# Performance work log

Hardware: AMD Instinct MI355X
Metric: run time of the kernel (lower is better)

Reference implementation:

```python
import jax, jax.numpy as jnp
import numpy as np

# Sampled-neighborhood sizes (NeighborSampler-style shrinking hops)
N0, N1, N2, N3 = 200000, 50000, 12500, 3200
E0, E1, E2 = 500000, 125000, 32000
D_IN, D_H, D_OUT = 128, 256, 128


def setup_inputs() -> dict:
    key = jax.random.key(0)
    ks = jax.random.split(key, 16)
    x = jax.random.normal(ks[0], (N0, D_IN), dtype=jnp.float32)
    src0 = jax.random.randint(ks[1], (E0,), 0, N0)
    dst0 = jax.random.randint(ks[2], (E0,), 0, N1)
    src1 = jax.random.randint(ks[3], (E1,), 0, N1)
    dst1 = jax.random.randint(ks[4], (E1,), 0, N2)
    src2 = jax.random.randint(ks[5], (E2,), 0, N2)
    dst2 = jax.random.randint(ks[6], (E2,), 0, N3)
    s = 0.05
    # SAGEConv params: lin_l (applied to aggregated neighbors, has bias), lin_r (root)
    wl0 = jax.random.normal(ks[7], (D_H, D_IN), dtype=jnp.float32) * s
    wr0 = jax.random.normal(ks[8], (D_H, D_IN), dtype=jnp.float32) * s
    b0 = jnp.zeros((D_H,), dtype=jnp.float32)
    wl1 = jax.random.normal(ks[9], (D_H, D_H), dtype=jnp.float32) * s
    wr1 = jax.random.normal(ks[10], (D_H, D_H), dtype=jnp.float32) * s
    b1 = jnp.zeros((D_H,), dtype=jnp.float32)
    wl2 = jax.random.normal(ks[11], (D_OUT, D_H), dtype=jnp.float32) * s
    wr2 = jax.random.normal(ks[12], (D_OUT, D_H), dtype=jnp.float32) * s
    b2 = jnp.zeros((D_OUT,), dtype=jnp.float32)
    return {"x": x, "src0": src0, "dst0": dst0, "src1": src1, "dst1": dst1,
            "src2": src2, "dst2": dst2,
            "wl0": wl0, "wr0": wr0, "b0": b0,
            "wl1": wl1, "wr1": wr1, "b1": b1,
            "wl2": wl2, "wr2": wr2, "b2": b2}


def _sage(x, src, dst, n_tgt, wl, wr, b):
    """Bipartite SAGEConv with mean aggregation (PyG default)."""
    x_tgt = x[:n_tgt]                                   # [n_tgt, d_in]
    msg = x[src]                                        # [E, d_in] gather
    s = jax.ops.segment_sum(msg, dst, num_segments=n_tgt)
    cnt = jax.ops.segment_sum(jnp.ones((src.shape[0], 1), x.dtype), dst,
                              num_segments=n_tgt)
    mean = s / jnp.maximum(cnt, 1.0)                    # mean over in-neighbors
    return mean @ wl.T + b + x_tgt @ wr.T               # [n_tgt, d_out]


def reference(x, src0, dst0, src1, dst1, src2, dst2,
              wl0, wr0, b0, wl1, wr1, b1, wl2, wr2, b2):
    h = jax.nn.relu(_sage(x, src0, dst0, N1, wl0, wr0, b0))
    h = jax.nn.relu(_sage(h, src1, dst1, N2, wl1, wr1, b1))
    return _sage(h, src2, dst2, N3, wl2, wr2, b2)       # [N3, D_OUT]
```

## Files before the change

kernel.cpp:

```cpp
#include <hip/hip_runtime.h>

#define N0s 200000
#define N1s 50000
#define N2s 12500
#define N3s 3200
#define E0s 500000
#define E1s 125000
#define E2s 32000
#define D_INs 128
#define D_Hs 256
#define D_OUTs 128

#define CAP 64
#define LOGCAP 6

#define GSTRIDE 72

#define XS4 (N1s * D_INs / 4)
#define WN4 65536
#define CSMALL_TOTAL (XS4 + WN4)
#define CSMALL_BLOCKS ((CSMALL_TOTAL + 2047) / 2048)

typedef __attribute__((ext_vector_type(8))) short short8;
typedef __attribute__((ext_vector_type(8))) unsigned short ushort8;
typedef __attribute__((ext_vector_type(4))) float floatx4;

__device__ __forceinline__ unsigned short f32_to_bf16_rne(float f) {
    unsigned int u = __float_as_uint(f);
    u += 0x7fffu + ((u >> 16) & 1u);
    return (unsigned short)(u >> 16);
}
__device__ __forceinline__ float bf16_to_f32(unsigned short h) {
    return __uint_as_float(((unsigned int)h) << 16);
}

struct Bins {
    const int *src0, *dst0, *src1, *dst1, *src2, *dst2;
    int *cnt0, *cnt1, *cnt2;
    int *eidx0, *eidx1, *eidx2;
};

__launch_bounds__(256)
__global__ void fill3(Bins b)
{
    int e = blockIdx.x * 256 + threadIdx.x;
    if (e < E0s) {
        int d = b.dst0[e];
        int p = atomicAdd(&b.cnt0[d], 1);
        if (p < CAP) b.eidx0[(d << LOGCAP) + p] = b.src0[e];
    } else if (e < E0s + E1s) {
        int i = e - E0s;
        int d = b.dst1[i];
        int p = atomicAdd(&b.cnt1[d], 1);
        if (p < CAP) b.eidx1[(d << LOGCAP) + p] = b.src1[i];
    } else if (e < E0s + E1s + E2s) {
        int i = e - E0s - E1s;
        int d = b.dst2[i];
        int p = atomicAdd(&b.cnt2[d], 1);
        if (p < CAP) b.eidx2[(d << LOGCAP) + p] = b.src2[i];
    }
}

struct CastArgs {
    const float* x; unsigned short* xb;
    const float* ws_[6]; unsigned short* wd[6];
};

__launch_bounds__(256)
__global__ void cast_small(CastArgs a)
{
    #pragma unroll
    for (int j = 0; j < 8; ++j) {
        int i = blockIdx.x * 2048 + j * 256 + threadIdx.x;
        if (i < XS4) {
            float4 v = *(const float4*)&a.x[(size_t)i * 4];
            ushort4 o;
            o.x = f32_to_bf16_rne(v.x);
            o.y = f32_to_bf16_rne(v.y);
            o.z = f32_to_bf16_rne(v.z);
            o.w = f32_to_bf16_rne(v.w);
            *(ushort4*)&a.xb[(size_t)i * 4] = o;
        } else if (i < CSMALL_TOTAL) {
            int g = i - XS4;
            int seg, base;
            if      (g < 8192)  { seg = 0; base = 0; }
            else if (g < 16384) { seg = 1; base = 8192; }
            else if (g < 32768) { seg = 2; base = 16384; }
            else if (g < 49152) { seg = 3; base = 32768; }
            else if (g < 57344) { seg = 4; base = 49152; }
            else                { seg = 5; base = 57344; }
            int k = g - base;
            float4 v = *(const float4*)&a.ws_[seg][(size_t)k * 4];
            ushort4 o;
            o.x = f32_to_bf16_rne(v.x);
            o.y = f32_to_bf16_rne(v.y);
            o.z = f32_to_bf16_rne(v.z);
            o.w = f32_to_bf16_rne(v.w);
            *(ushort4*)&a.wd[seg][(size_t)k * 4] = o;
        }
    }
}

__launch_bounds__(256)
__global__ void gather_mean_f32(const float* __restrict__ X,
                                const int* __restrict__ eidx,
                                const int* __restrict__ cnt,
                                unsigned short* __restrict__ out,
                                int n_tgt)
{
    int gid = blockIdx.x * 256 + threadIdx.x;
    int row = gid >> 5;
    if (row >= n_tgt) return;
    int c = (gid & 31) << 2;

    int deg = cnt[row];
    int e = min(deg, CAP);
    const int* bp = &eidx[row << LOGCAP];

    float a0 = 0.f, a1 = 0.f, a2 = 0.f, a3 = 0.f;
    int i = 0;
    for (; i + 4 <= e; i += 4) {
        int4 ss = *(const int4*)&bp[i];
        float4 v0 = *(const float4*)&X[(size_t)ss.x * D_INs + c];
        float4 v1 = *(const float4*)&X[(size_t)ss.y * D_INs + c];
        float4 v2 = *(const float4*)&X[(size_t)ss.z * D_INs + c];
        float4 v3 = *(const float4*)&X[(size_t)ss.w * D_INs + c];
        a0 += (v0.x + v1.x) + (v2.x + v3.x);
        a1 += (v0.y + v1.y) + (v2.y + v3.y);
        a2 += (v0.z + v1.z) + (v2.z + v3.z);
        a3 += (v0.w + v1.w) + (v2.w + v3.w);
    }
    for (; i < e; ++i) {
        float4 v = *(const float4*)&X[(size_t)bp[i] * D_INs + c];
        a0 += v.x; a1 += v.y; a2 += v.z; a3 += v.w;
    }
    float inv = 1.0f / fmaxf((float)deg, 1.0f);
    ushort4 o;
    o.x = f32_to_bf16_rne(a0 * inv);
    o.y = f32_to_bf16_rne(a1 * inv);
    o.z = f32_to_bf16_rne(a2 * inv);
    o.w = f32_to_bf16_rne(a3 * inv);
    *(ushort4*)&out[(size_t)row * D_INs + c] = o;
}

__launch_bounds__(256)
__global__ void gather_mean(const unsigned short* __restrict__ X,
                            const int* __restrict__ eidx,
                            const int* __restrict__ cnt,
                            unsigned short* __restrict__ out,
                            int n_tgt, int D, int shift)
{
    int gid = blockIdx.x * 256 + threadIdx.x;
    int row = gid >> shift;
    if (row >= n_tgt) return;
    int c = (gid & ((1 << shift) - 1)) << 3;

    int deg = cnt[row];
    int e = min(deg, CAP);
    const int* bp = &eidx[row << LOGCAP];

    float acc[8];
    #pragma unroll
    for (int j = 0; j < 8; ++j) acc[j] = 0.f;

    int i = 0;
    for (; i + 4 <= e; i += 4) {
        int4 ss = *(const int4*)&bp[i];
        ushort8 v0 = *(const ushort8*)&X[(size_t)ss.x * D + c];
        ushort8 v1 = *(const ushort8*)&X[(size_t)ss.y * D + c];
        ushort8 v2 = *(const ushort8*)&X[(size_t)ss.z * D + c];
        ushort8 v3 = *(const ushort8*)&X[(size_t)ss.w * D + c];
        #pragma unroll
        for (int j = 0; j < 8; ++j)
            acc[j] += (bf16_to_f32(v0[j]) + bf16_to_f32(v1[j]))
                    + (bf16_to_f32(v2[j]) + bf16_to_f32(v3[j]));
    }
    for (; i < e; ++i) {
        ushort8 v0 = *(const ushort8*)&X[(size_t)bp[i] * D + c];
        #pragma unroll
        for (int j = 0; j < 8; ++j) acc[j] += bf16_to_f32(v0[j]);
    }

    float inv = 1.0f / fmaxf((float)deg, 1.0f);
    ushort8 o;
    #pragma unroll
    for (int j = 0; j < 8; ++j) o[j] = f32_to_bf16_rne(acc[j] * inv);
    *(ushort8*)&out[(size_t)row * D + c] = o;
}

template<int BM, int BN, int OUT_BF16, int RELU>
__launch_bounds__(256)
__global__ void mfma_gemm_t(const unsigned short* __restrict__ A1,
                            const unsigned short* __restrict__ A2,
                            const unsigned short* __restrict__ W1,
                            const unsigned short* __restrict__ W2,
                            const float* __restrict__ bias,
                            void* __restrict__ Cout,
                            int M, int N, int K1, int K2)
{
    constexpr int MT = BM / 32;
    constexpr int NT = BN / 32;
    constexpr int AITER = BM / 32;
    constexpr int CS = BN + 4;

    __shared__ unsigned short smem[2 * BM * GSTRIDE];
    unsigned short* As = smem;
    unsigned short* Bs = smem + BM * GSTRIDE;

    const int tid  = threadIdx.x;
    const int wave = tid >> 6;
    const int lane = tid & 63;
    const int quad = lane >> 4;
    const int lr   = lane & 15;
    const int wm   = wave >> 1;
    const int wn   = wave & 1;
    const int row0 = blockIdx.x * BM;
    const int col0 = blockIdx.y * BN;

    floatx4 acc[MT][NT] = {};

    for (int seg = 0; seg < 2; ++seg) {
        const unsigned short* Ap = (seg == 0) ? A1 : A2;
        const unsigned short* Wp = (seg == 0) ? W1 : W2;
        const int K = (seg == 0) ? K1 : K2;

        for (int k0 = 0; k0 < K; k0 += 64) {
            #pragma unroll
            for (int it = 0; it < AITER; ++it) {
                int sid = tid + it * 256;
                int r = sid >> 3;
                int sc = (sid & 7) << 3;
                int gr = min(row0 + r, M - 1);
                uint4 v = *(const uint4*)&Ap[(size_t)gr * K + k0 + sc];
                *(uint4*)&As[r * GSTRIDE + sc] = v;
            }
            #pragma unroll
            for (int it = 0; it < AITER; ++it) {
                int sid = tid + it * 256;
                int r = sid >> 3;
                int sc = (sid & 7) << 3;
                uint4 v = *(const uint4*)&Wp[(size_t)(col0 + r) * K + k0 + sc];
                *(uint4*)&Bs[r * GSTRIDE + sc] = v;
            }
            __syncthreads();

            #pragma unroll
            for (int kh = 0; kh < 2; ++kh) {
                short8 afr[MT], bfr[NT];
                #pragma unroll
                for (int mt = 0; mt < MT; ++mt)
                    afr[mt] = *(const short8*)&As[(wm * (BM/2) + mt * 16 + lr) * GSTRIDE + kh * 32 + quad * 8];
                #pragma unroll
                for (int nt = 0; nt < NT; ++nt)
                    bfr[nt] = *(const short8*)&Bs[(wn * (BN/2) + nt * 16 + lr) * GSTRIDE + kh * 32 + quad * 8];

                #pragma unroll
                for (int mt = 0; mt < MT; ++mt)
                    #pragma unroll
                    for (int nt = 0; nt < NT; ++nt)
                        acc[mt][nt] = __builtin_amdgcn_mfma_f32_16x16x32_bf16(
                            afr[mt], bfr[nt], acc[mt][nt], 0, 0, 0);
            }
            __syncthreads();
        }
    }

    if (OUT_BF16) {
        unsigned short* Cs = smem;
        #pragma unroll
        for (int nt = 0; nt < NT; ++nt) {
            int col = wn * (BN/2) + nt * 16 + lr;
            float bv = bias[col0 + col];
            #pragma unroll
            for (int mt = 0; mt < MT; ++mt) {
                #pragma unroll
                for (int reg = 0; reg < 4; ++reg) {
                    int row = wm * (BM/2) + mt * 16 + quad * 4 + reg;
                    float v = acc[mt][nt][reg] + bv;
                    if (RELU) v = fmaxf(v, 0.f);
                    Cs[row * CS + col] = f32_to_bf16_rne(v);
                }
            }
        }
        __syncthreads();
        constexpr int TPRO = 256 / BM;
        constexpr int SPT  = BN / TPRO;
        int r  = tid / TPRO;
        int hf = tid % TPRO;
        int gr = row0 + r;
        if (gr < M) {
            unsigned short* Crow = (unsigned short*)Cout + (size_t)gr * N + col0 + hf * SPT;
            #pragma unroll
            for (int j = 0; j < SPT / 8; ++j) {
                uint4 v = *(const uint4*)&Cs[r * CS + hf * SPT + j * 8];
                *(uint4*)&Crow[j * 8] = v;
            }
        }
    } else {
        #pragma unroll
        for (int nt = 0; nt < NT; ++nt) {
            int gc = col0 + wn * (BN/2) + nt * 16 + lr;
            float bv = bias[gc];
            #pragma unroll
            for (int mt = 0; mt < MT; ++mt) {
                #pragma unroll
                for (int reg = 0; reg < 4; ++reg) {
                    int gr = row0 + wm * (BM/2) + mt * 16 + quad * 4 + reg;
                    if (gr < M) {
                        float v = acc[mt][nt][reg] + bv;
                        if (RELU) v = fmaxf(v, 0.f);
                        ((float*)Cout)[(size_t)gr * N + gc] = v;
                    }
                }
            }
        }
    }
}

extern "C" void kernel_launch(void* const* d_in, const int* in_sizes, int n_in,
                              void* d_out, int out_size, void* d_ws, size_t ws_size,
                              hipStream_t stream)
{
    const float* x   = (const float*)d_in[0];
    const int* src0  = (const int*)d_in[1];
    const int* dst0  = (const int*)d_in[2];
    const int* src1  = (const int*)d_in[3];
    const int* dst1  = (const int*)d_in[4];
    const int* src2  = (const int*)d_in[5];
    const int* dst2  = (const int*)d_in[6];
    const float* wl0 = (const float*)d_in[7];
    const float* wr0 = (const float*)d_in[8];
    const float* b0  = (const float*)d_in[9];
    const float* wl1 = (const float*)d_in[10];
    const float* wr1 = (const float*)d_in[11];
    const float* b1  = (const float*)d_in[12];
    const float* wl2 = (const float*)d_in[13];
    const float* wr2 = (const float*)d_in[14];
    const float* b2  = (const float*)d_in[15];

    unsigned short* ws = (unsigned short*)d_ws;
    unsigned short* xb    = ws;
    unsigned short* h1    = xb + (size_t)N0s * D_INs;
    unsigned short* h2    = h1 + (size_t)N1s * D_Hs;
    unsigned short* meanA = h2 + (size_t)N2s * D_Hs;
    unsigned short* wl0b  = meanA + (size_t)N1s * D_INs;
    unsigned short* wr0b  = wl0b + 32768;
    unsigned short* wl1b  = wr0b + 32768;
    unsigned short* wr1b  = wl1b + 65536;
    unsigned short* wl2b  = wr1b + 65536;
    unsigned short* wr2b  = wl2b + 32768;
    int* ib = (int*)(wr2b + 32768);
    int* cnt0 = ib;
    int* cnt1 = cnt0 + 50048;
    int* cnt2 = cnt1 + 12544;
    int* eidx0 = cnt2 + 3264;
    int* eidx1 = eidx0 + (size_t)N1s * CAP;
    int* eidx2 = eidx1 + (size_t)N2s * CAP;

    Bins b;
    b.src0 = src0; b.dst0 = dst0; b.src1 = src1; b.dst1 = dst1;
    b.src2 = src2; b.dst2 = dst2;
    b.cnt0 = cnt0; b.cnt1 = cnt1; b.cnt2 = cnt2;
    b.eidx0 = eidx0; b.eidx1 = eidx1; b.eidx2 = eidx2;

    CastArgs ca;
    ca.x = x; ca.xb = xb;
    ca.ws_[0] = wl0; ca.ws_[1] = wr0; ca.ws_[2] = wl1;
    ca.ws_[3] = wr1; ca.ws_[4] = wl2; ca.ws_[5] = wr2;
    ca.wd[0] = wl0b; ca.wd[1] = wr0b; ca.wd[2] = wl1b;
    ca.wd[3] = wr1b; ca.wd[4] = wl2b; ca.wd[5] = wr2b;

    hipMemsetAsync(cnt0, 0, (50048 + 12544 + 3264) * sizeof(int), stream);
    const int Etot = E0s + E1s + E2s;
    fill3<<<(Etot + 255) / 256, 256, 0, stream>>>(b);
    cast_small<<<CSMALL_BLOCKS, 256, 0, stream>>>(ca);

    {
        int th = N1s * 32;
        gather_mean_f32<<<(th + 255) / 256, 256, 0, stream>>>(x, eidx0, cnt0,
                                                              meanA, N1s);
        dim3 g((N1s + 127) / 128, D_Hs / 128);
        mfma_gemm_t<128,128,1,1><<<g, 256, 0, stream>>>(meanA, xb, wl0b, wr0b, b0, h1,
                                                        N1s, D_Hs, D_INs, D_INs);
    }
    {
        int th = N2s * 32;
        gather_mean<<<(th + 255) / 256, 256, 0, stream>>>(h1, eidx1, cnt1,
                                                          meanA, N2s, D_Hs, 5);
        dim3 g((N2s + 63) / 64, D_Hs / 64);
        mfma_gemm_t<64,64,1,1><<<g, 256, 0, stream>>>(meanA, h1, wl1b, wr1b, b1, h2,
                                                      N2s, D_Hs, D_Hs, D_Hs);
    }
    {
        int th = N3s * 32;
        gather_mean<<<(th + 255) / 256, 256, 0, stream>>>(h2, eidx2, cnt2,
                                                          meanA, N3s, D_Hs, 5);
        dim3 g((N3s + 63) / 64, D_OUTs / 64);
        mfma_gemm_t<64,64,0,0><<<g, 256, 0, stream>>>(meanA, h2, wl2b, wr2b, b2, (float*)d_out,
                                                      N3s, D_OUTs, D_Hs, D_Hs);
    }
}
```

Before: 317.9 us.

## Fuse cast with layer-0 gather and widen GEMM tiles to full output width

Merges the bf16 cast kernel and the fp32 layer-0 gather-mean into one launch, splitting the grid between the two jobs, so one launch and one serialization point go away and the two can overlap. The GEMM template now supports BN different from BM, with separate A and B load iteration counts and shared memory sized to the max of the staging buffers and the output tile. Each layer's GEMM uses a full-width N tile (128x256, 64x256, 32x128), so the A operand is read once instead of once per column block. Wider tiles use more registers and shared memory and launch fewer blocks, which may lower occupancy, most of all on the small later layers.

```diff
diff --git a/kernel.cpp b/kernel.cpp
--- a/kernel.cpp
+++ b/kernel.cpp
@@ -20,6 +20,7 @@
 #define WN4 65536
 #define CSMALL_TOTAL (XS4 + WN4)
 #define CSMALL_BLOCKS ((CSMALL_TOTAL + 2047) / 2048)
+#define G0_BLOCKS (N1s * 32 / 256)
 
 typedef __attribute__((ext_vector_type(8))) short short8;
 typedef __attribute__((ext_vector_type(8))) unsigned short ushort8;
@@ -61,77 +62,73 @@
     }
 }
 
-struct CastArgs {
+struct G0Args {
     const float* x; unsigned short* xb;
     const float* ws_[6]; unsigned short* wd[6];
+    const int* eidx0; const int* cnt0; unsigned short* meanA;
 };
 
 __launch_bounds__(256)
-__global__ void cast_small(CastArgs a)
+__global__ void gather0_cast(G0Args a)
 {
-    #pragma unroll
-    for (int j = 0; j < 8; ++j) {
-        int i = blockIdx.x * 2048 + j * 256 + threadIdx.x;
-        if (i < XS4) {
-            float4 v = *(const float4*)&a.x[(size_t)i * 4];
-            ushort4 o;
-            o.x = f32_to_bf16_rne(v.x);
-            o.y = f32_to_bf16_rne(v.y);
-            o.z = f32_to_bf16_rne(v.z);
-            o.w = f32_to_bf16_rne(v.w);
-            *(ushort4*)&a.xb[(size_t)i * 4] = o;
-        } else if (i < CSMALL_TOTAL) {
-            int g = i - XS4;
-            int seg, base;
-            if      (g < 8192)  { seg = 0; base = 0; }
-            else if (g < 16384) { seg = 1; base = 8192; }
-            else if (g < 32768) { seg = 2; base = 16384; }
-            else if (g < 49152) { seg = 3; base = 32768; }
-            else if (g < 57344) { seg = 4; base = 49152; }
-            else                { seg = 5; base = 57344; }
-            int k = g - base;
-            float4 v = *(const float4*)&a.ws_[seg][(size_t)k * 4];
-            ushort4 o;
-            o.x = f32_to_bf16_rne(v.x);
-            o.y = f32_to_bf16_rne(v.y);
-            o.z = f32_to_bf16_rne(v.z);
-            o.w = f32_to_bf16_rne(v.w);
-            *(ushort4*)&a.wd[seg][(size_t)k * 4] = o;
+    if (blockIdx.x < CSMALL_BLOCKS) {
+        #pragma unroll
+        for (int j = 0; j < 8; ++j) {
+            int i = blockIdx.x * 2048 + j * 256 + threadIdx.x;
+            if (i < XS4) {
+                float4 v = *(const float4*)&a.x[(size_t)i * 4];
+                ushort4 o;
+                o.x = f32_to_bf16_rne(v.x);
+                o.y = f32_to_bf16_rne(v.y);
+                o.z = f32_to_bf16_rne(v.z);
+                o.w = f32_to_bf16_rne(v.w);
+                *(ushort4*)&a.xb[(size_t)i * 4] = o;
+            } else if (i < CSMALL_TOTAL) {
+                int g = i - XS4;
+                int seg, base;
+                if      (g < 8192)  { seg = 0; base = 0; }
+                else if (g < 16384) { seg = 1; base = 8192; }
+                else if (g < 32768) { seg = 2; base = 16384; }
+                else if (g < 49152) { seg = 3; base = 32768; }
+                else if (g < 57344) { seg = 4; base = 49152; }
+                else                { seg = 5; base = 57344; }
+                int k = g - base;
+                float4 v = *(const float4*)&a.ws_[seg][(size_t)k * 4];
+                ushort4 o;
+                o.x = f32_to_bf16_rne(v.x);
+                o.y = f32_to_bf16_rne(v.y);
+                o.z = f32_to_bf16_rne(v.z);
+                o.w = f32_to_bf16_rne(v.w);
+                *(ushort4*)&a.wd[seg][(size_t)k * 4] = o;
+            }
         }
-    }
-}
-
-__launch_bounds__(256)
-__global__ void gather_mean_f32(const float* __restrict__ X,
-                                const int* __restrict__ eidx,
-                                const int* __restrict__ cnt,
-                                unsigned short* __restrict__ out,
-                                int n_tgt)
-{
-    int gid = blockIdx.x * 256 + threadIdx.x;
+        return;
+    }
+
+    int gid = (blockIdx.x - CSMALL_BLOCKS) * 256 + threadIdx.x;
     int row = gid >> 5;
-    if (row >= n_tgt) return;
+    if (row >= N1s) return;
     int c = (gid & 31) << 2;
 
-    int deg = cnt[row];
+    int deg = a.cnt0[row];
     int e = min(deg, CAP);
-    const int* bp = &eidx[row << LOGCAP];
+    const int* bp = &a.eidx0[row << LOGCAP];
 
     float a0 = 0.f, a1 = 0.f, a2 = 0.f, a3 = 0.f;
     int i = 0;
     for (; i + 4 <= e; i += 4) {
         int4 ss = *(const int4*)&bp[i];
-        float4 v0 = *(const float4*)&X[(size_t)ss.x * D_INs + c];
-        float4 v1 = *(const float4*)&X[(size_t)ss.y * D_INs + c];
-        float4 v2 = *(const float4*)&X[(size_t)ss.z * D_INs + c];
-        float4 v3 = *(const float4*)&X[(size_t)ss.w * D_INs + c];
+        float4 v0 = *(const float4*)&a.x[(size_t)ss.x * D_INs + c];
+        float4 v1 = *(const float4*)&a.x[(size_t)ss.y * D_INs + c];
+        float4 v2 = *(const float4*)&a.x[(size_t)ss.z * D_INs + c];
+        float4 v3 = *(const float4*)&a.x[(size_t)ss.w * D_INs + c];
         a0 += (v0.x + v1.x) + (v2.x + v3.x);
         a1 += (v0.y + v1.y) + (v2.y + v3.y);
         a2 += (v0.z + v1.z) + (v2.z + v3.z);
         a3 += (v0.w + v1.w) + (v2.w + v3.w);
     }
     for (; i < e; ++i) {
-        float4 v = *(const float4*)&X[(size_t)bp[i] * D_INs + c];
+        float4 v = *(const float4*)&a.x[(size_t)bp[i] * D_INs + c];
         a0 += v.x; a1 += v.y; a2 += v.z; a3 += v.w;
     }
     float inv = 1.0f / fmaxf((float)deg, 1.0f);
@@ -140,7 +137,7 @@
     o.y = f32_to_bf16_rne(a1 * inv);
     o.z = f32_to_bf16_rne(a2 * inv);
     o.w = f32_to_bf16_rne(a3 * inv);
-    *(ushort4*)&out[(size_t)row * D_INs + c] = o;
+    *(ushort4*)&a.meanA[(size_t)row * D_INs + c] = o;
 }
 
 __launch_bounds__(256)
@@ -200,10 +197,14 @@
 {
     constexpr int MT = BM / 32;
     constexpr int NT = BN / 32;
-    constexpr int AITER = BM / 32;
+    constexpr int AITER_A = BM / 32;
+    constexpr int AITER_B = BN / 32;
     constexpr int CS = BN + 4;
-
-    __shared__ unsigned short smem[2 * BM * GSTRIDE];
+    constexpr int STAGE_SH = (BM + BN) * GSTRIDE;
+    constexpr int CS_SH = OUT_BF16 ? BM * CS : 0;
+    constexpr int SMEM_SH = STAGE_SH > CS_SH ? STAGE_SH : CS_SH;
+
+    __shared__ unsigned short smem[SMEM_SH];
     unsigned short* As = smem;
     unsigned short* Bs = smem + BM * GSTRIDE;
 
@@ -226,7 +227,7 @@
 
         for (int k0 = 0; k0 < K; k0 += 64) {
             #pragma unroll
-            for (int it = 0; it < AITER; ++it) {
+            for (int it = 0; it < AITER_A; ++it) {
                 int sid = tid + it * 256;
                 int r = sid >> 3;
                 int sc = (sid & 7) << 3;
@@ -235,7 +236,7 @@
                 *(uint4*)&As[r * GSTRIDE + sc] = v;
             }
             #pragma unroll
-            for (int it = 0; it < AITER; ++it) {
+            for (int it = 0; it < AITER_B; ++it) {
                 int sid = tid + it * 256;
                 int r = sid >> 3;
                 int sc = (sid & 7) << 3;
@@ -363,40 +364,38 @@
     b.cnt0 = cnt0; b.cnt1 = cnt1; b.cnt2 = cnt2;
     b.eidx0 = eidx0; b.eidx1 = eidx1; b.eidx2 = eidx2;
 
-    CastArgs ca;
-    ca.x = x; ca.xb = xb;
-    ca.ws_[0] = wl0; ca.ws_[1] = wr0; ca.ws_[2] = wl1;
-    ca.ws_[3] = wr1; ca.ws_[4] = wl2; ca.ws_[5] = wr2;
-    ca.wd[0] = wl0b; ca.wd[1] = wr0b; ca.wd[2] = wl1b;
-    ca.wd[3] = wr1b; ca.wd[4] = wl2b; ca.wd[5] = wr2b;
+    G0Args ga;
+    ga.x = x; ga.xb = xb;
+    ga.ws_[0] = wl0; ga.ws_[1] = wr0; ga.ws_[2] = wl1;
+    ga.ws_[3] = wr1; ga.ws_[4] = wl2; ga.ws_[5] = wr2;
+    ga.wd[0] = wl0b; ga.wd[1] = wr0b; ga.wd[2] = wl1b;
+    ga.wd[3] = wr1b; ga.wd[4] = wl2b; ga.wd[5] = wr2b;
+    ga.eidx0 = eidx0; ga.cnt0 = cnt0; ga.meanA = meanA;
 
     hipMemsetAsync(cnt0, 0, (50048 + 12544 + 3264) * sizeof(int), stream);
     const int Etot = E0s + E1s + E2s;
     fill3<<<(Etot + 255) / 256, 256, 0, stream>>>(b);
-    cast_small<<<CSMALL_BLOCKS, 256, 0, stream>>>(ca);
-
+
+    gather0_cast<<<CSMALL_BLOCKS + G0_BLOCKS, 256, 0, stream>>>(ga);
     {
-        int th = N1s * 32;
-        gather_mean_f32<<<(th + 255) / 256, 256, 0, stream>>>(x, eidx0, cnt0,
-                                                              meanA, N1s);
-        dim3 g((N1s + 127) / 128, D_Hs / 128);
-        mfma_gemm_t<128,128,1,1><<<g, 256, 0, stream>>>(meanA, xb, wl0b, wr0b, b0, h1,
+        dim3 g((N1s + 127) / 128, 1);
+        mfma_gemm_t<128,256,1,1><<<g, 256, 0, stream>>>(meanA, xb, wl0b, wr0b, b0, h1,
                                                         N1s, D_Hs, D_INs, D_INs);
     }
     {
         int th = N2s * 32;
         gather_mean<<<(th + 255) / 256, 256, 0, stream>>>(h1, eidx1, cnt1,
                                                           meanA, N2s, D_Hs, 5);
-        dim3 g((N2s + 63) / 64, D_Hs / 64);
-        mfma_gemm_t<64,64,1,1><<<g, 256, 0, stream>>>(meanA, h1, wl1b, wr1b, b1, h2,
-                                                      N2s, D_Hs, D_Hs, D_Hs);
+        dim3 g((N2s + 63) / 64, 1);
+        mfma_gemm_t<64,256,1,1><<<g, 256, 0, stream>>>(meanA, h1, wl1b, wr1b, b1, h2,
+                                                       N2s, D_Hs, D_Hs, D_Hs);
     }
     {
         int th = N3s * 32;
         gather_mean<<<(th + 255) / 256, 256, 0, stream>>>(h2, eidx2, cnt2,
                                                           meanA, N3s, D_Hs, 5);
-        dim3 g((N3s + 63) / 64, D_OUTs / 64);
-        mfma_gemm_t<64,64,0,0><<<g, 256, 0, stream>>>(meanA, h2, wl2b, wr2b, b2, (float*)d_out,
-                                                      N3s, D_OUTs, D_Hs, D_Hs);
-    }
-}
+        dim3 g((N3s + 31) / 32, 1);
+        mfma_gemm_t<32,128,0,0><<<g, 256, 0, stream>>>(meanA, h2, wl2b, wr2b, b2, (float*)d_out,
+                                                       N3s, D_OUTs, D_Hs, D_Hs);
+    }
+}
```

Measured after the change: 338.8 us. 6.6% more time.
